# Kernel tuning notes

Measured on AMD Instinct MI355X. Metric: run time of the kernel, lower is better.

## Reference

```python
import jax, jax.numpy as jnp
from jax import lax
import numpy as np

EPS = 1e-5


def _fps(xyz, S):
    B, N, _ = xyz.shape

    def step(carry, _):
        dist, far = carry  # [B,N], [B]
        c = xyz[jnp.arange(B), far]               # [B,3]
        d = jnp.sum((xyz - c[:, None, :]) ** 2, -1)  # [B,N]
        dist = jnp.minimum(dist, d)
        nxt = jnp.argmax(dist, -1).astype(jnp.int32)
        return (dist, nxt), far

    init = (jnp.full((B, N), 1e10, xyz.dtype), jnp.zeros((B,), jnp.int32))
    _, idxs = lax.scan(step, init, None, length=S)
    return jnp.transpose(idxs)  # [B,S]


def _gather(pts, idx):
    # pts: [B,N,C], idx: [B,...] -> [B,...,C]
    return jax.vmap(lambda p, i: p[i])(pts, idx)


def _conv(x, W, b):
    # 1x1 Conv1d: x [M,Cin,L], W [Cout,Cin], b [Cout]
    return jnp.einsum('mcl,oc->mol', x, W) + b[None, :, None]


def _bn(x, g, b):
    # BatchNorm1d (training-mode batch stats, biased variance)
    mu = jnp.mean(x, (0, 2), keepdims=True)
    v = jnp.var(x, (0, 2), keepdims=True)
    return g[None, :, None] * (x - mu) / jnp.sqrt(v + EPS) + b[None, :, None]


def _forward(xyz, feature, affine_alpha, affine_beta, w_tr, b_tr, g_tr, be_tr,
             w1, b1, g1, be1, w2, b2, groups, k):
    xyz = jnp.transpose(xyz, (0, 2, 1))        # [B,N,3]
    feature = jnp.transpose(feature, (0, 2, 1))  # [B,N,D]
    B, N, _ = xyz.shape
    S = groups
    xyz_ng = lax.stop_gradient(xyz)  # cluster() runs under torch.no_grad
    fps_idx = _fps(xyz_ng, S)                        # [B,S]
    new_xyz = _gather(xyz_ng, fps_idx)               # [B,S,3] (detached)
    # squared-distance kNN: [B,S,N]
    sqr = (jnp.sum(new_xyz ** 2, -1)[:, :, None]
           + jnp.sum(xyz_ng ** 2, -1)[:, None, :]
           - 2.0 * jnp.einsum('bsc,bnc->bsn', new_xyz, xyz_ng))
    _, idx = lax.top_k(-sqr, k)                      # [B,S,k] smallest distances
    new_feature = _gather(feature, fps_idx)          # [B,S,D]
    grouped_xyz = _gather(xyz, idx)                  # [B,S,k,3]
    grouped_feature = _gather(feature, idx)          # [B,S,k,D]
    grouped_feature = jnp.concatenate([grouped_feature, grouped_xyz], -1)  # [B,S,k,D+3]
    # anchor normalization
    mean = jnp.concatenate([new_feature, new_xyz], -1)[:, :, None, :]  # [B,S,1,D+3]
    diff = grouped_feature - mean
    std = jnp.std(diff.reshape(B, -1), axis=-1, ddof=1)[:, None, None, None]
    gf = affine_alpha * (diff / (std + EPS)) + affine_beta
    # concat anchor feature -> [B,S,k,2D+3]
    D = new_feature.shape[-1]
    x = jnp.concatenate([gf, jnp.broadcast_to(new_feature[:, :, None, :], (B, S, k, D))], -1)
    d = x.shape[-1]
    # PreExtraction: [B,S,k,d] -> [B*S,d,k]
    x = jnp.transpose(x, (0, 1, 3, 2)).reshape(B * S, d, k)
    x = jax.nn.relu(_bn(_conv(x, w_tr, b_tr), g_tr, be_tr))
    y = jax.nn.relu(_bn(_conv(x, w1, b1), g1, be1))
    y = _conv(y, w2, b2)
    x = jax.nn.relu(y + x)
    x = jnp.max(x, -1).reshape(B, S, -1)             # adaptive_max_pool1d(1)
    return (jnp.transpose(new_xyz, (0, 2, 1)), jnp.transpose(x, (0, 2, 1)))


def setup_inputs() -> dict:
    key = jax.random.key(0)
    k0, k1, k2, k3, k4 = jax.random.split(key, 5)
    B, N, D = 8, 4096, 64
    return {
        'xyz': jax.random.normal(k0, (B, 3, N), jnp.float32),
        'feature': jax.random.normal(k1, (B, D, N), jnp.float32),
        'affine_alpha': jnp.ones((1, 1, 1, D + 3), jnp.float32),
        'affine_beta': jnp.zeros((1, 1, 1, D + 3), jnp.float32),
        'w_tr': 0.05 * jax.random.normal(k2, (D, 3 + 2 * D), jnp.float32),
        'b_tr': jnp.zeros((D,), jnp.float32),
        'g_tr': jnp.ones((D,), jnp.float32),
        'be_tr': jnp.zeros((D,), jnp.float32),
        'w1': 0.05 * jax.random.normal(k3, (D, D), jnp.float32),
        'b1': jnp.zeros((D,), jnp.float32),
        'g1': jnp.ones((D,), jnp.float32),
        'be1': jnp.zeros((D,), jnp.float32),
        'w2': 0.05 * jax.random.normal(k4, (D, D), jnp.float32),
        'b2': jnp.zeros((D,), jnp.float32),
        'groups': 1024,
        'k': 32,
    }


def reference(xyz, feature, affine_alpha, affine_beta, w_tr, b_tr, g_tr, be_tr,
              w1, b1, g1, be1, w2, b2, groups, k):
    return _forward(xyz, feature, affine_alpha, affine_beta, w_tr, b_tr, g_tr, be_tr,
                    w1, b1, g1, be1, w2, b2, groups, k)
```

## Files before the change

kernel.cpp:

```cpp
#include <hip/hip_runtime.h>
#include <cfloat>
#include <math.h>

#define B_ 8
#define N_ 4096
#define D_ 64
#define S_ 1024
#define K_ 32
#define CIN_ 131

template <int CTRL>
__device__ __forceinline__ unsigned long long dpp_u64(unsigned long long k) {
  int lo = (int)(unsigned int)k, hi = (int)(unsigned int)(k >> 32);
  lo = __builtin_amdgcn_update_dpp(lo, lo, CTRL, 0xf, 0xf, false);
  hi = __builtin_amdgcn_update_dpp(hi, hi, CTRL, 0xf, 0xf, false);
  return ((unsigned long long)(unsigned int)hi << 32) | (unsigned int)lo;
}

__device__ __forceinline__ float wave_max_f32_dpp(float v) {
  int x = __float_as_int(v);
#define STEP(ctrl)                                                        \
  {                                                                       \
    int t = __builtin_amdgcn_update_dpp(x, x, ctrl, 0xf, 0xf, false);     \
    v = fmaxf(v, __int_as_float(t));                                      \
    x = __float_as_int(v);                                                \
  }
  STEP(0x111)
  STEP(0x112)
  STEP(0x114)
  STEP(0x118)
  STEP(0x142)
  STEP(0x143)
#undef STEP
  return __int_as_float(__builtin_amdgcn_readlane(x, 63));
}

__global__ __launch_bounds__(512) void fps_kernel(const float* __restrict__ xyz,
                                                  int* __restrict__ fps_idx,
                                                  float* __restrict__ nxyz,
                                                  float* __restrict__ out0) {
  const int b = blockIdx.x, tid = threadIdx.x;
  __shared__ __align__(16) float4 sp[N_];
  __shared__ int si[S_];
  __shared__ unsigned long long keyp[2][8];
  const float* xb = xyz + (size_t)b * 3 * N_;
  const float4* xv = (const float4*)xb;
  float px[8], py[8], pz[8], dist[8];
  {
    float4 x0 = xv[2 * tid], x1 = xv[2 * tid + 1];
    float4 y0 = xv[1024 + 2 * tid], y1 = xv[1024 + 2 * tid + 1];
    float4 z0 = xv[2048 + 2 * tid], z1 = xv[2048 + 2 * tid + 1];
    px[0] = x0.x; px[1] = x0.y; px[2] = x0.z; px[3] = x0.w;
    px[4] = x1.x; px[5] = x1.y; px[6] = x1.z; px[7] = x1.w;
    py[0] = y0.x; py[1] = y0.y; py[2] = y0.z; py[3] = y0.w;
    py[4] = y1.x; py[5] = y1.y; py[6] = y1.z; py[7] = y1.w;
    pz[0] = z0.x; pz[1] = z0.y; pz[2] = z0.z; pz[3] = z0.w;
    pz[4] = z1.x; pz[5] = z1.y; pz[6] = z1.z; pz[7] = z1.w;
#pragma unroll
    for (int i = 0; i < 8; i++) {
      dist[i] = 1e10f;
      sp[8 * tid + i] = make_float4(px[i], py[i], pz[i], 0.f);
    }
  }
  if (tid == 0) si[0] = 0;
  __syncthreads();
  float cx = sp[0].x, cy = sp[0].y, cz = sp[0].z;
  const int wav = tid >> 6, lane = tid & 63;
  for (int s = 1; s < S_; s++) {
    float best = -1.0f;
    int bi = 8 * tid;
#pragma unroll
    for (int i = 0; i < 8; i++) {
      float dx = __fsub_rn(px[i], cx);
      float dy = __fsub_rn(py[i], cy);
      float dz = __fsub_rn(pz[i], cz);
      float d = __fadd_rn(__fadd_rn(__fmul_rn(dx, dx), __fmul_rn(dy, dy)), __fmul_rn(dz, dz));
      dist[i] = fminf(dist[i], d);
      if (dist[i] > best) { best = dist[i]; bi = 8 * tid + i; }
    }
    float wmax = wave_max_f32_dpp(best);
    unsigned long long m = __ballot(best == wmax);
    int l = __ffsll(m) - 1;
    int widx = __builtin_amdgcn_readlane(bi, l);
    if (lane == 0)
      keyp[s & 1][wav] =
          ((unsigned long long)(unsigned int)__float_as_int(wmax) << 32) |
          (unsigned int)(4095 - widx);
    __syncthreads();
    unsigned long long k = keyp[s & 1][lane & 7];
    unsigned long long t;
    t = dpp_u64<0xB1>(k);  if (t > k) k = t;
    t = dpp_u64<0x4E>(k);  if (t > k) k = t;
    t = dpp_u64<0x124>(k); if (t > k) k = t;
    int bix = 4095 - (int)(k & 0xfffull);
    if (tid == 0) si[s] = bix;
    float4 c = sp[bix];
    cx = c.x; cy = c.y; cz = c.z;
  }
  __syncthreads();
  for (int e = tid; e < S_; e += 512) {
    int n = si[e];
    fps_idx[b * S_ + e] = n;
    float4 c = sp[n];
    nxyz[(size_t)(b * S_ + e) * 3 + 0] = c.x;
    nxyz[(size_t)(b * S_ + e) * 3 + 1] = c.y;
    nxyz[(size_t)(b * S_ + e) * 3 + 2] = c.z;
    out0[(size_t)b * 3 * S_ + e] = c.x;
    out0[(size_t)b * 3 * S_ + S_ + e] = c.y;
    out0[(size_t)b * 3 * S_ + 2 * S_ + e] = c.z;
  }
}

__global__ __launch_bounds__(256) void knn_kernel(const float* __restrict__ xyz,
                                                  const float* __restrict__ nxyz,
                                                  int* __restrict__ knn) {
  const int bs = blockIdx.x, tid = threadIdx.x;
  const int b = bs >> 10;
  const float* xb = xyz + (size_t)b * 3 * N_;
  const float cx = nxyz[(size_t)bs * 3], cy = nxyz[(size_t)bs * 3 + 1], cz = nxyz[(size_t)bs * 3 + 2];
  const float cn = __fadd_rn(__fadd_rn(__fmul_rn(cx, cx), __fmul_rn(cy, cy)), __fmul_rn(cz, cz));
  float d[16];
#pragma unroll
  for (int i = 0; i < 16; i++) {
    int n = i * 256 + tid;
    float px = xb[n], py = xb[N_ + n], pz = xb[2 * N_ + n];
    float pn = __fadd_rn(__fadd_rn(__fmul_rn(px, px), __fmul_rn(py, py)), __fmul_rn(pz, pz));
    float dot = __fadd_rn(__fadd_rn(__fmul_rn(cx, px), __fmul_rn(cy, py)), __fmul_rn(cz, pz));
    d[i] = __fsub_rn(__fadd_rn(cn, pn), __fmul_rn(2.0f, dot));
  }
  float mv = FLT_MAX;
  int mi = tid;
#pragma unroll
  for (int i = 0; i < 16; i++)
    if (d[i] < mv) { mv = d[i]; mi = i * 256 + tid; }
  __shared__ unsigned long long keyp[2][4];
  __shared__ int skk[K_];
  const int wav = tid >> 6, lane = tid & 63;
  for (int j = 0; j < K_; j++) {
    unsigned int u = __float_as_uint(mv);
    u ^= ((unsigned int)((int)u >> 31) | 0x80000000u);
    unsigned long long key = ((unsigned long long)u << 32) | (unsigned int)mi;
#pragma unroll
    for (int off = 32; off >= 1; off >>= 1) {
      unsigned long long ok = __shfl_xor(key, off);
      if (ok < key) key = ok;
    }
    if (lane == 0) keyp[j & 1][wav] = key;
    __syncthreads();
    unsigned long long kmin = keyp[j & 1][0];
#pragma unroll
    for (int w = 1; w < 4; w++) {
      unsigned long long k2 = keyp[j & 1][w];
      if (k2 < kmin) kmin = k2;
    }
    int g = (int)(kmin & 0xffffffffull);
    if (tid == 0) skk[j] = g;
    if ((g & 255) == tid) {
      int sl = g >> 8;
#pragma unroll
      for (int i = 0; i < 16; i++)
        if (i == sl) d[i] = FLT_MAX;
      mv = FLT_MAX; mi = tid;
#pragma unroll
      for (int i = 0; i < 16; i++)
        if (d[i] < mv) { mv = d[i]; mi = i * 256 + tid; }
    }
  }
  __syncthreads();
  if (tid < K_) knn[(size_t)bs * K_ + tid] = skk[tid];
}

__global__ __launch_bounds__(256) void gather_nf(const float* __restrict__ feature,
                                                 const int* __restrict__ fps_i,
                                                 float* __restrict__ nfeat) {
  int e = blockIdx.x * 256 + threadIdx.x;
  int b = e >> 16, rem = e & 65535;
  int s = rem >> 6, c = rem & 63;
  int n = fps_i[b * S_ + s];
  nfeat[e] = feature[((size_t)b * 64 + c) * N_ + n];
}

__global__ __launch_bounds__(256) void std_partial(const float* __restrict__ feature,
                                                   const float* __restrict__ xyz,
                                                   const float* __restrict__ nxyz,
                                                   const float* __restrict__ nfeat,
                                                   const int* __restrict__ knn,
                                                   float* __restrict__ outp) {
  const int blk = blockIdx.x, tid = threadIdx.x;
  const int b = blk >> 6, chunk = blk & 63;
  float s = 0.f, q = 0.f;
  for (int e = tid; e < 16 * K_ * 67; e += 256) {
    int so = e / (K_ * 67);
    int rem = e - so * (K_ * 67);
    int kk = rem / 67;
    int c = rem - kk * 67;
    int bs = b * S_ + chunk * 16 + so;
    int n = knn[(size_t)bs * K_ + kk];
    float raw = (c < 64) ? feature[((size_t)b * 64 + c) * N_ + n]
                         : xyz[((size_t)b * 3 + (c - 64)) * N_ + n];
    float anc = (c < 64) ? nfeat[(size_t)bs * 64 + c]
                         : nxyz[(size_t)bs * 3 + (c - 64)];
    float dd = raw - anc;
    s += dd; q += dd * dd;
  }
#pragma unroll
  for (int off = 32; off >= 1; off >>= 1) { s += __shfl_xor(s, off); q += __shfl_xor(q, off); }
  __shared__ float rs[4], rq[4];
  if ((tid & 63) == 0) { rs[tid >> 6] = s; rq[tid >> 6] = q; }
  __syncthreads();
  if (tid == 0) {
    outp[blk * 2] = rs[0] + rs[1] + rs[2] + rs[3];
    outp[blk * 2 + 1] = rq[0] + rq[1] + rq[2] + rq[3];
  }
}

__global__ void std_final(const float* __restrict__ part, float* __restrict__ invstd) {
  int b = threadIdx.x;
  if (b < B_) {
    double s = 0.0, q = 0.0;
    for (int i = 0; i < 64; i++) {
      s += (double)part[(b * 64 + i) * 2];
      q += (double)part[(b * 64 + i) * 2 + 1];
    }
    const double n = (double)(S_ * K_ * 67);
    double var = (q - s * s / n) / (n - 1.0);
    invstd[b] = (float)(1.0 / (sqrt(var) + 1e-5));
  }
}

template <int MODE>
__global__ __launch_bounds__(256, 2) void mlp_kernel(
    const float* __restrict__ feature, const float* __restrict__ xyz,
    const float* __restrict__ nxyz, const float* __restrict__ nfeat,
    const int* __restrict__ knn, const float* __restrict__ invstd,
    const float* __restrict__ alpha, const float* __restrict__ beta,
    const float* __restrict__ w_tr, const float* __restrict__ b_tr,
    const float* __restrict__ w1, const float* __restrict__ b1,
    const float* __restrict__ w2, const float* __restrict__ b2,
    const float* __restrict__ bn_tr, const float* __restrict__ bn_1,
    float* __restrict__ bnpart, float* __restrict__ out1) {
  __shared__ __align__(16) float pool[15556];
  float* Wt = pool;
  float* xin = pool + 8516;
  float* ub = xin;
  float* tb = pool + 8516 + 4192;
  float* part = pool + 8516 + 4192 + 2304;
  int* sknn = (int*)(part + 512);
  const int bs = blockIdx.x, tid = threadIdx.x;
  const int b = bs >> 10, s = bs & 1023;
  if (tid < K_) sknn[tid] = knn[(size_t)bs * K_ + tid];
  for (int e = tid; e < 64 * 131; e += 256) {
    int o = e / 131, c = e - o * 131;
    Wt[c * 65 + o] = w_tr[e];
  }
  __syncthreads();
  const float inv = invstd[b];
  for (int e = tid; e < CIN_ * K_; e += 256) {
    int c = e >> 5, kk = e & 31;
    float v;
    if (c < 67) {
      int n = sknn[kk];
      float raw = (c < 64) ? feature[((size_t)b * 64 + c) * N_ + n]
                           : xyz[((size_t)b * 3 + (c - 64)) * N_ + n];
      float anc = (c < 64) ? nfeat[(size_t)bs * 64 + c]
                           : nxyz[(size_t)bs * 3 + (c - 64)];
      v = alpha[c] * ((raw - anc) * inv) + beta[c];
    } else {
      v = nfeat[(size_t)bs * 64 + (c - 67)];
    }
    xin[e] = v;
  }
  __syncthreads();
  const int o = tid & 63, kkb = (tid >> 6) * 8;
  float acc[8];
  {
    float bv = b_tr[o];
#pragma unroll
    for (int j = 0; j < 8; j++) acc[j] = bv;
  }
  for (int c = 0; c < CIN_; c++) {
    float w = Wt[c * 65 + o];
    const float4 xa = *(const float4*)(xin + c * 32 + kkb);
    const float4 xb4 = *(const float4*)(xin + c * 32 + kkb + 4);
    acc[0] += w * xa.x; acc[1] += w * xa.y; acc[2] += w * xa.z; acc[3] += w * xa.w;
    acc[4] += w * xb4.x; acc[5] += w * xb4.y; acc[6] += w * xb4.z; acc[7] += w * xb4.w;
  }
  if (MODE == 0) {
    float s8 = 0.f, q8 = 0.f;
#pragma unroll
    for (int j = 0; j < 8; j++) { s8 += acc[j]; q8 += acc[j] * acc[j]; }
    part[(tid >> 6) * 64 + o] = s8;
    part[256 + (tid >> 6) * 64 + o] = q8;
    __syncthreads();
    if (tid < 64) {
      float ss = 0.f, qq = 0.f;
      for (int g = 0; g < 4; g++) { ss += part[g * 64 + tid]; qq += part[256 + g * 64 + tid]; }
      bnpart[(size_t)bs * 128 + tid] = ss;
      bnpart[(size_t)bs * 128 + 64 + tid] = qq;
    }
    return;
  }
  float tv[8];
  {
    float sc = bn_tr[o], sh = bn_tr[64 + o];
#pragma unroll
    for (int j = 0; j < 8; j++) {
      tv[j] = fmaxf(fmaf(sc, acc[j], sh), 0.f);
      tb[o * 36 + kkb + j] = tv[j];
    }
  }
  __syncthreads();
  for (int e = tid; e < 64 * 64; e += 256) {
    int oo = e >> 6, c = e & 63;
    Wt[c * 65 + oo] = w1[e];
  }
  __syncthreads();
  float acc2[8];
  {
    float bv = b1[o];
#pragma unroll
    for (int j = 0; j < 8; j++) acc2[j] = bv;
  }
  for (int c = 0; c < 64; c++) {
    float w = Wt[c * 65 + o];
    const float4 ta = *(const float4*)(tb + c * 36 + kkb);
    const float4 ta2 = *(const float4*)(tb + c * 36 + kkb + 4);
    acc2[0] += w * ta.x; acc2[1] += w * ta.y; acc2[2] += w * ta.z; acc2[3] += w * ta.w;
    acc2[4] += w * ta2.x; acc2[5] += w * ta2.y; acc2[6] += w * ta2.z; acc2[7] += w * ta2.w;
  }
  if (MODE == 1) {
    float s8 = 0.f, q8 = 0.f;
#pragma unroll
    for (int j = 0; j < 8; j++) { s8 += acc2[j]; q8 += acc2[j] * acc2[j]; }
    part[(tid >> 6) * 64 + o] = s8;
    part[256 + (tid >> 6) * 64 + o] = q8;
    __syncthreads();
    if (tid < 64) {
      float ss = 0.f, qq = 0.f;
      for (int g = 0; g < 4; g++) { ss += part[g * 64 + tid]; qq += part[256 + g * 64 + tid]; }
      bnpart[(size_t)bs * 128 + tid] = ss;
      bnpart[(size_t)bs * 128 + 64 + tid] = qq;
    }
    return;
  }
  {
    float sc = bn_1[o], sh = bn_1[64 + o];
#pragma unroll
    for (int j = 0; j < 8; j++) ub[o * 36 + kkb + j] = fmaxf(fmaf(sc, acc2[j], sh), 0.f);
  }
  __syncthreads();
  for (int e = tid; e < 64 * 64; e += 256) {
    int oo = e >> 6, c = e & 63;
    Wt[c * 65 + oo] = w2[e];
  }
  __syncthreads();
  float acc3[8];
  {
    float bv = b2[o];
#pragma unroll
    for (int j = 0; j < 8; j++) acc3[j] = bv;
  }
  for (int c = 0; c < 64; c++) {
    float w = Wt[c * 65 + o];
    const float4 ua = *(const float4*)(ub + c * 36 + kkb);
    const float4 ua2 = *(const float4*)(ub + c * 36 + kkb + 4);
    acc3[0] += w * ua.x; acc3[1] += w * ua.y; acc3[2] += w * ua.z; acc3[3] += w * ua.w;
    acc3[4] += w * ua2.x; acc3[5] += w * ua2.y; acc3[6] += w * ua2.z; acc3[7] += w * ua2.w;
  }
  float m = 0.f;
#pragma unroll
  for (int j = 0; j < 8; j++) m = fmaxf(m, fmaxf(acc3[j] + tv[j], 0.f));
  part[(tid >> 6) * 64 + o] = m;
  __syncthreads();
  if (tid < 64) {
    float mm = part[tid];
    for (int g = 1; g < 4; g++) mm = fmaxf(mm, part[g * 64 + tid]);
    out1[((size_t)b * 64 + tid) * S_ + s] = mm;
  }
}

__global__ __launch_bounds__(256) void bn_finalize(const float* __restrict__ part,
                                                   const float* __restrict__ g,
                                                   const float* __restrict__ be,
                                                   float* __restrict__ bnout) {
  const int ch = blockIdx.x, tid = threadIdx.x;
  double s = 0.0, q = 0.0;
  for (int i = tid; i < B_ * S_; i += 256) {
    s += (double)part[(size_t)i * 128 + ch];
    q += (double)part[(size_t)i * 128 + 64 + ch];
  }
#pragma unroll
  for (int off = 32; off >= 1; off >>= 1) { s += __shfl_xor(s, off); q += __shfl_xor(q, off); }
  __shared__ double ls[4], lq[4];
  if ((tid & 63) == 0) { ls[tid >> 6] = s; lq[tid >> 6] = q; }
  __syncthreads();
  if (tid == 0) {
    double Ssum = ls[0] + ls[1] + ls[2] + ls[3];
    double Qsum = lq[0] + lq[1] + lq[2] + lq[3];
    const double n = (double)(B_ * S_ * K_);
    double mu = Ssum / n;
    double var = Qsum / n - mu * mu;
    double sc = (double)g[ch] / sqrt(var + 1e-5);
    bnout[ch] = (float)sc;
    bnout[64 + ch] = (float)((double)be[ch] - mu * sc);
  }
}


__global__ __launch_bounds__(256) void transpose_feat(const float* __restrict__ feature,
                                                      float* __restrict__ featT) {
  __shared__ float tile[64 * 65];
  const int blk = blockIdx.x, tid = threadIdx.x;
  const int b = blk >> 6, n0 = (blk & 63) * 64;
#pragma unroll
  for (int i = 0; i < 16; i++) {
    int c = i * 4 + (tid >> 6), nl = tid & 63;
    tile[c * 65 + nl] = feature[((size_t)b * 64 + c) * N_ + n0 + nl];
  }
  __syncthreads();
#pragma unroll
  for (int i = 0; i < 16; i++) {
    int nl = i * 4 + (tid >> 6), c = tid & 63;
    featT[((size_t)b * N_ + n0 + nl) * 64 + c] = tile[c * 65 + nl];
  }
}

__global__ __launch_bounds__(256) void gather_nf_c(const float* __restrict__ featT,
                                                   const int* __restrict__ fps_i,
                                                   float* __restrict__ nfeat) {
  int e = blockIdx.x * 256 + threadIdx.x;
  int bs = e >> 6, c = e & 63;
  int b = bs >> 10;
  int n = fps_i[bs];
  nfeat[e] = featT[((size_t)b * N_ + n) * 64 + c];
}

__global__ __launch_bounds__(256) void prep_kernel(const float* __restrict__ featT,
                                                   const float* __restrict__ xyz,
                                                   const float* __restrict__ nxyz,
                                                   const float* __restrict__ nfeat,
                                                   const int* __restrict__ knn,
                                                   float* __restrict__ dcache,
                                                   float* __restrict__ outp) {
  const int blk = blockIdx.x, tid = threadIdx.x;
  __shared__ int sk[32];
  float s = 0.f, q = 0.f;
  const int c = tid & 63, qd = tid >> 6;
  for (int g = 0; g < 8; g++) {
    const int bs = blk * 8 + g, b = bs >> 10;
    if (tid < 32) sk[tid] = knn[(size_t)bs * K_ + tid];
    __syncthreads();
    float anc = nfeat[(size_t)bs * 64 + c];
#pragma unroll
    for (int it = 0; it < 8; it++) {
      int kk = it * 4 + qd;
      int n = sk[kk];
      float dd = featT[((size_t)b * N_ + n) * 64 + c] - anc;
      s += dd; q += dd * dd;
      dcache[((size_t)bs * 32 + kk) * 68 + c] = dd;
    }
    if (tid < 96) {
      int c3 = tid >> 5, kk = tid & 31;
      int n = sk[kk];
      float dd = xyz[((size_t)b * 3 + c3) * N_ + n] - nxyz[(size_t)bs * 3 + c3];
      s += dd; q += dd * dd;
      dcache[((size_t)bs * 32 + kk) * 68 + 64 + c3] = dd;
    }
    __syncthreads();
  }
#pragma unroll
  for (int off = 32; off >= 1; off >>= 1) { s += __shfl_xor(s, off); q += __shfl_xor(q, off); }
  __shared__ float rs[4], rq[4];
  if ((tid & 63) == 0) { rs[tid >> 6] = s; rq[tid >> 6] = q; }
  __syncthreads();
  if (tid == 0) {
    outp[blk * 2] = rs[0] + rs[1] + rs[2] + rs[3];
    outp[blk * 2 + 1] = rq[0] + rq[1] + rq[2] + rq[3];
  }
}

__global__ void std_final_c(const float* __restrict__ part, float* __restrict__ invstd) {
  int b = threadIdx.x;
  if (b < B_) {
    double s = 0.0, q = 0.0;
    for (int i = 0; i < 128; i++) {
      s += (double)part[(b * 128 + i) * 2];
      q += (double)part[(b * 128 + i) * 2 + 1];
    }
    const double n = (double)(S_ * K_ * 67);
    double var = (q - s * s / n) / (n - 1.0);
    invstd[b] = (float)(1.0 / (sqrt(var) + 1e-5));
  }
}

__global__ __launch_bounds__(256, 2) void mlp0c(
    const float* __restrict__ dcache, const float* __restrict__ nfeat,
    const float* __restrict__ invstd,
    const float* __restrict__ alpha, const float* __restrict__ beta,
    const float* __restrict__ w_tr, const float* __restrict__ b_tr,
    float* __restrict__ bnpart, float* __restrict__ tcache) {
  __shared__ __align__(16) float pool[13220];
  float* Wt = pool;
  float* xin = pool + 8516;
  float* part = pool + 8516 + 4192;
  const int bs = blockIdx.x, tid = threadIdx.x;
  const int b = bs >> 10;
  for (int e = tid; e < 64 * 131; e += 256) {
    int o = e / 131, c = e - o * 131;
    Wt[c * 65 + o] = w_tr[e];
  }
  const float inv = invstd[b];
  {
    const int c = tid & 63, qd = tid >> 6;
    float al = alpha[c], bev = beta[c];
#pragma unroll
    for (int it = 0; it < 8; it++) {
      int kk = it * 4 + qd;
      xin[c * 32 + kk] = al * (dcache[((size_t)bs * 32 + kk) * 68 + c] * inv) + bev;
    }
    if (tid < 96) {
      int c3 = 64 + (tid >> 5), kk = tid & 31;
      xin[c3 * 32 + kk] =
          alpha[c3] * (dcache[((size_t)bs * 32 + kk) * 68 + c3] * inv) + beta[c3];
    }
    for (int e = tid; e < 2048; e += 256) {
      int cc = 67 + (e >> 5), kk = e & 31;
      xin[cc * 32 + kk] = nfeat[(size_t)bs * 64 + (e >> 5)];
    }
  }
  __syncthreads();
  const int o = tid & 63, kkb = (tid >> 6) * 8;
  float acc[8];
  {
    float bv = b_tr[o];
#pragma unroll
    for (int j = 0; j < 8; j++) acc[j] = bv;
  }
  for (int c = 0; c < CIN_; c++) {
    float w = Wt[c * 65 + o];
    const float4 xa = *(const float4*)(xin + c * 32 + kkb);
    const float4 xb4 = *(const float4*)(xin + c * 32 + kkb + 4);
    acc[0] += w * xa.x; acc[1] += w * xa.y; acc[2] += w * xa.z; acc[3] += w * xa.w;
    acc[4] += w * xb4.x; acc[5] += w * xb4.y; acc[6] += w * xb4.z; acc[7] += w * xb4.w;
  }
  {
    float4* tp = (float4*)(tcache + ((size_t)bs * 64 + o) * 32 + kkb);
    tp[0] = make_float4(acc[0], acc[1], acc[2], acc[3]);
    tp[1] = make_float4(acc[4], acc[5], acc[6], acc[7]);
  }
  float s8 = 0.f, q8 = 0.f;
#pragma unroll
  for (int j = 0; j < 8; j++) { s8 += acc[j]; q8 += acc[j] * acc[j]; }
  part[(tid >> 6) * 64 + o] = s8;
  part[256 + (tid >> 6) * 64 + o] = q8;
  __syncthreads();
  if (tid < 64) {
    float ss = 0.f, qq = 0.f;
    for (int g = 0; g < 4; g++) { ss += part[g * 64 + tid]; qq += part[256 + g * 64 + tid]; }
    bnpart[(size_t)bs * 128 + tid] = ss;
    bnpart[(size_t)bs * 128 + 64 + tid] = qq;
  }
}

__global__ __launch_bounds__(256, 3) void mlp1c(
    const float* __restrict__ tcache, const float* __restrict__ bn_tr,
    const float* __restrict__ w1, const float* __restrict__ b1,
    float* __restrict__ bnpart, float* __restrict__ ucache) {
  __shared__ __align__(16) float pool[6976];
  float* Wt = pool;
  float* tb = pool + 4160;
  float* part = pool + 4160 + 2304;
  const int bs = blockIdx.x, tid = threadIdx.x;
  const int o = tid & 63, kkb = (tid >> 6) * 8;
  for (int e = tid; e < 64 * 64; e += 256) {
    int oo = e >> 6, c = e & 63;
    Wt[c * 65 + oo] = w1[e];
  }
  float t[8];
  {
    const float4* tp = (const float4*)(tcache + ((size_t)bs * 64 + o) * 32 + kkb);
    float4 a = tp[0], b4 = tp[1];
    t[0] = a.x; t[1] = a.y; t[2] = a.z; t[3] = a.w;
    t[4] = b4.x; t[5] = b4.y; t[6] = b4.z; t[7] = b4.w;
  }
  {
    float sc = bn_tr[o], sh = bn_tr[64 + o];
#pragma unroll
    for (int j = 0; j < 8; j++) tb[o * 36 + kkb + j] = fmaxf(fmaf(sc, t[j], sh), 0.f);
  }
  __syncthreads();
  float acc2[8];
  {
    float bv = b1[o];
#pragma unroll
    for (int j = 0; j < 8; j++) acc2[j] = bv;
  }
  for (int c = 0; c < 64; c++) {
    float w = Wt[c * 65 + o];
    const float4 ta = *(const float4*)(tb + c * 36 + kkb);
    const float4 ta2 = *(const float4*)(tb + c * 36 + kkb + 4);
    acc2[0] += w * ta.x; acc2[1] += w * ta.y; acc2[2] += w * ta.z; acc2[3] += w * ta.w;
    acc2[4] += w * ta2.x; acc2[5] += w * ta2.y; acc2[6] += w * ta2.z; acc2[7] += w * ta2.w;
  }
  {
    float4* up = (float4*)(ucache + ((size_t)bs * 64 + o) * 32 + kkb);
    up[0] = make_float4(acc2[0], acc2[1], acc2[2], acc2[3]);
    up[1] = make_float4(acc2[4], acc2[5], acc2[6], acc2[7]);
  }
  float s8 = 0.f, q8 = 0.f;
#pragma unroll
  for (int j = 0; j < 8; j++) { s8 += acc2[j]; q8 += acc2[j] * acc2[j]; }
  part[(tid >> 6) * 64 + o] = s8;
  part[256 + (tid >> 6) * 64 + o] = q8;
  __syncthreads();
  if (tid < 64) {
    float ss = 0.f, qq = 0.f;
    for (int g = 0; g < 4; g++) { ss += part[g * 64 + tid]; qq += part[256 + g * 64 + tid]; }
    bnpart[(size_t)bs * 128 + tid] = ss;
    bnpart[(size_t)bs * 128 + 64 + tid] = qq;
  }
}

__global__ __launch_bounds__(256, 3) void mlp2c(
    const float* __restrict__ tcache, const float* __restrict__ ucache,
    const float* __restrict__ bn_tr, const float* __restrict__ bn_1,
    const float* __restrict__ w2, const float* __restrict__ b2,
    float* __restrict__ out1) {
  __shared__ __align__(16) float pool[6976];
  float* Wt = pool;
  float* ub = pool + 4160;
  float* part = pool + 4160 + 2304;
  const int bs = blockIdx.x, tid = threadIdx.x;
  const int b = bs >> 10, s = bs & 1023;
  const int o = tid & 63, kkb = (tid >> 6) * 8;
  for (int e = tid; e < 64 * 64; e += 256) {
    int oo = e >> 6, c = e & 63;
    Wt[c * 65 + oo] = w2[e];
  }
  {
    const float4* up = (const float4*)(ucache + ((size_t)bs * 64 + o) * 32 + kkb);
    float4 a = up[0], b4 = up[1];
    float u[8] = {a.x, a.y, a.z, a.w, b4.x, b4.y, b4.z, b4.w};
    float sc = bn_1[o], sh = bn_1[64 + o];
#pragma unroll
    for (int j = 0; j < 8; j++) ub[o * 36 + kkb + j] = fmaxf(fmaf(sc, u[j], sh), 0.f);
  }
  __syncthreads();
  float acc3[8];
  {
    float bv = b2[o];
#pragma unroll
    for (int j = 0; j < 8; j++) acc3[j] = bv;
  }
  for (int c = 0; c < 64; c++) {
    float w = Wt[c * 65 + o];
    const float4 ua = *(const float4*)(ub + c * 36 + kkb);
    const float4 ua2 = *(const float4*)(ub + c * 36 + kkb + 4);
    acc3[0] += w * ua.x; acc3[1] += w * ua.y; acc3[2] += w * ua.z; acc3[3] += w * ua.w;
    acc3[4] += w * ua2.x; acc3[5] += w * ua2.y; acc3[6] += w * ua2.z; acc3[7] += w * ua2.w;
  }
  float tv[8];
  {
    const float4* tp = (const float4*)(tcache + ((size_t)bs * 64 + o) * 32 + kkb);
    float4 a = tp[0], b4 = tp[1];
    float t[8] = {a.x, a.y, a.z, a.w, b4.x, b4.y, b4.z, b4.w};
    float sc = bn_tr[o], sh = bn_tr[64 + o];
#pragma unroll
    for (int j = 0; j < 8; j++) tv[j] = fmaxf(fmaf(sc, t[j], sh), 0.f);
  }
  float m = 0.f;
#pragma unroll
  for (int j = 0; j < 8; j++) m = fmaxf(m, fmaxf(acc3[j] + tv[j], 0.f));
  part[(tid >> 6) * 64 + o] = m;
  __syncthreads();
  if (tid < 64) {
    float mm = part[tid];
    for (int g = 1; g < 4; g++) mm = fmaxf(mm, part[g * 64 + tid]);
    out1[((size_t)b * 64 + tid) * S_ + s] = mm;
  }
}

extern "C" void kernel_launch(void* const* d_in, const int* in_sizes, int n_in,
                              void* d_out, int out_size, void* d_ws, size_t ws_size,
                              hipStream_t stream) {
  const float* xyz = (const float*)d_in[0];
  const float* feature = (const float*)d_in[1];
  const float* alpha = (const float*)d_in[2];
  const float* beta = (const float*)d_in[3];
  const float* w_tr = (const float*)d_in[4];
  const float* b_tr = (const float*)d_in[5];
  const float* g_tr = (const float*)d_in[6];
  const float* be_tr = (const float*)d_in[7];
  const float* w1 = (const float*)d_in[8];
  const float* b1 = (const float*)d_in[9];
  const float* g1 = (const float*)d_in[10];
  const float* be1 = (const float*)d_in[11];
  const float* w2 = (const float*)d_in[12];
  const float* b2 = (const float*)d_in[13];

  char* ws = (char*)d_ws;
  int* fps_i = (int*)(ws);
  float* nxyz = (float*)(ws + 32768);
  float* nfeat = (float*)(ws + 131072);
  int* knn = (int*)(ws + 2228224);
  float* stdpart = (float*)(ws + 3276800);
  float* invstd = (float*)(ws + 3280896);
  float* bn_tr = (float*)(ws + 3280960);
  float* bn_1 = (float*)(ws + 3281472);
  float* bnpart = (float*)(ws + 3281984);
  float* featT = (float*)(ws + 7476288);
  float* dcache = (float*)(ws + 15864896);
  float* tcache = (float*)(ws + 87168064);
  float* ucache = (float*)(ws + 154276928);
  float* stdpart_c = (float*)(ws + 221385792);

  float* out0 = (float*)d_out;
  float* out1 = out0 + B_ * 3 * S_;

  const bool big = (ws_size >= 221393984ull);

  fps_kernel<<<B_, 512, 0, stream>>>(xyz, fps_i, nxyz, out0);

  if (big) {
    transpose_feat<<<8 * 64, 256, 0, stream>>>(feature, featT);
    knn_kernel<<<B_ * S_, 256, 0, stream>>>(xyz, nxyz, knn);
    gather_nf_c<<<(B_ * S_ * D_) / 256, 256, 0, stream>>>(featT, fps_i, nfeat);
    prep_kernel<<<1024, 256, 0, stream>>>(featT, xyz, nxyz, nfeat, knn, dcache, stdpart_c);
    std_final_c<<<1, 64, 0, stream>>>(stdpart_c, invstd);
    mlp0c<<<B_ * S_, 256, 0, stream>>>(dcache, nfeat, invstd, alpha, beta, w_tr, b_tr,
                                       bnpart, tcache);
    bn_finalize<<<64, 256, 0, stream>>>(bnpart, g_tr, be_tr, bn_tr);
    mlp1c<<<B_ * S_, 256, 0, stream>>>(tcache, bn_tr, w1, b1, bnpart, ucache);
    bn_finalize<<<64, 256, 0, stream>>>(bnpart, g1, be1, bn_1);
    mlp2c<<<B_ * S_, 256, 0, stream>>>(tcache, ucache, bn_tr, bn_1, w2, b2, out1);
  } else {
    gather_nf<<<(B_ * S_ * D_) / 256, 256, 0, stream>>>(feature, fps_i, nfeat);
    knn_kernel<<<B_ * S_, 256, 0, stream>>>(xyz, nxyz, knn);
    std_partial<<<B_ * 64, 256, 0, stream>>>(feature, xyz, nxyz, nfeat, knn, stdpart);
    std_final<<<1, 64, 0, stream>>>(stdpart, invstd);
    mlp_kernel<0><<<B_ * S_, 256, 0, stream>>>(feature, xyz, nxyz, nfeat, knn, invstd,
                                               alpha, beta, w_tr, b_tr, w1, b1, w2, b2,
                                               bn_tr, bn_1, bnpart, out1);
    bn_finalize<<<64, 256, 0, stream>>>(bnpart, g_tr, be_tr, bn_tr);
    mlp_kernel<1><<<B_ * S_, 256, 0, stream>>>(feature, xyz, nxyz, nfeat, knn, invstd,
                                               alpha, beta, w_tr, b_tr, w1, b1, w2, b2,
                                               bn_tr, bn_1, bnpart, out1);
    bn_finalize<<<64, 256, 0, stream>>>(bnpart, g1, be1, bn_1);
    mlp_kernel<2><<<B_ * S_, 256, 0, stream>>>(feature, xyz, nxyz, nfeat, knn, invstd,
                                               alpha, beta, w_tr, b_tr, w1, b1, w2, b2,
                                               bn_tr, bn_1, bnpart, out1);
  }
}
```

Baseline: 1.196 ms.

## Fuse feature transpose into FPS launch and gather into kNN launch, shrink FPS block

```diff
diff --git a/kernel.cpp b/kernel.cpp
--- a/kernel.cpp
+++ b/kernel.cpp
@@ -35,32 +35,50 @@
   return __int_as_float(__builtin_amdgcn_readlane(x, 63));
 }
 
-__global__ __launch_bounds__(512) void fps_kernel(const float* __restrict__ xyz,
+__global__ __launch_bounds__(256) void fps_kernel(const float* __restrict__ xyz,
                                                   int* __restrict__ fps_idx,
                                                   float* __restrict__ nxyz,
-                                                  float* __restrict__ out0) {
-  const int b = blockIdx.x, tid = threadIdx.x;
+                                                  float* __restrict__ out0,
+                                                  const float* __restrict__ feature,
+                                                  float* __restrict__ featT) {
+  const int tid = threadIdx.x;
   __shared__ __align__(16) float4 sp[N_];
   __shared__ int si[S_];
-  __shared__ unsigned long long keyp[2][8];
+  __shared__ unsigned long long keyp[2][4];
+  if (blockIdx.x >= 8) {
+    const int blk = blockIdx.x - 8;
+    const int b = blk >> 6, n0 = (blk & 63) * 64;
+    float* tile = (float*)sp;
+#pragma unroll
+    for (int i = 0; i < 16; i++) {
+      int c = i * 4 + (tid >> 6), nl = tid & 63;
+      tile[c * 65 + nl] = feature[((size_t)b * 64 + c) * N_ + n0 + nl];
+    }
+    __syncthreads();
+#pragma unroll
+    for (int i = 0; i < 16; i++) {
+      int nl = i * 4 + (tid >> 6), c = tid & 63;
+      featT[((size_t)b * N_ + n0 + nl) * 64 + c] = tile[c * 65 + nl];
+    }
+    return;
+  }
+  const int b = blockIdx.x;
   const float* xb = xyz + (size_t)b * 3 * N_;
   const float4* xv = (const float4*)xb;
-  float px[8], py[8], pz[8], dist[8];
-  {
-    float4 x0 = xv[2 * tid], x1 = xv[2 * tid + 1];
-    float4 y0 = xv[1024 + 2 * tid], y1 = xv[1024 + 2 * tid + 1];
-    float4 z0 = xv[2048 + 2 * tid], z1 = xv[2048 + 2 * tid + 1];
-    px[0] = x0.x; px[1] = x0.y; px[2] = x0.z; px[3] = x0.w;
-    px[4] = x1.x; px[5] = x1.y; px[6] = x1.z; px[7] = x1.w;
-    py[0] = y0.x; py[1] = y0.y; py[2] = y0.z; py[3] = y0.w;
-    py[4] = y1.x; py[5] = y1.y; py[6] = y1.z; py[7] = y1.w;
-    pz[0] = z0.x; pz[1] = z0.y; pz[2] = z0.z; pz[3] = z0.w;
-    pz[4] = z1.x; pz[5] = z1.y; pz[6] = z1.z; pz[7] = z1.w;
-#pragma unroll
-    for (int i = 0; i < 8; i++) {
-      dist[i] = 1e10f;
-      sp[8 * tid + i] = make_float4(px[i], py[i], pz[i], 0.f);
-    }
+  float px[16], py[16], pz[16], dist[16];
+#pragma unroll
+  for (int q = 0; q < 4; q++) {
+    float4 X = xv[4 * tid + q];
+    float4 Y = xv[1024 + 4 * tid + q];
+    float4 Z = xv[2048 + 4 * tid + q];
+    px[4 * q + 0] = X.x; px[4 * q + 1] = X.y; px[4 * q + 2] = X.z; px[4 * q + 3] = X.w;
+    py[4 * q + 0] = Y.x; py[4 * q + 1] = Y.y; py[4 * q + 2] = Y.z; py[4 * q + 3] = Y.w;
+    pz[4 * q + 0] = Z.x; pz[4 * q + 1] = Z.y; pz[4 * q + 2] = Z.z; pz[4 * q + 3] = Z.w;
+  }
+#pragma unroll
+  for (int i = 0; i < 16; i++) {
+    dist[i] = 1e10f;
+    sp[16 * tid + i] = make_float4(px[i], py[i], pz[i], 0.f);
   }
   if (tid == 0) si[0] = 0;
   __syncthreads();
@@ -68,15 +86,15 @@
   const int wav = tid >> 6, lane = tid & 63;
   for (int s = 1; s < S_; s++) {
     float best = -1.0f;
-    int bi = 8 * tid;
-#pragma unroll
-    for (int i = 0; i < 8; i++) {
+    int bi = 16 * tid;
+#pragma unroll
+    for (int i = 0; i < 16; i++) {
       float dx = __fsub_rn(px[i], cx);
       float dy = __fsub_rn(py[i], cy);
       float dz = __fsub_rn(pz[i], cz);
       float d = __fadd_rn(__fadd_rn(__fmul_rn(dx, dx), __fmul_rn(dy, dy)), __fmul_rn(dz, dz));
       dist[i] = fminf(dist[i], d);
-      if (dist[i] > best) { best = dist[i]; bi = 8 * tid + i; }
+      if (dist[i] > best) { best = dist[i]; bi = 16 * tid + i; }
     }
     float wmax = wave_max_f32_dpp(best);
     unsigned long long m = __ballot(best == wmax);
@@ -87,18 +105,17 @@
           ((unsigned long long)(unsigned int)__float_as_int(wmax) << 32) |
           (unsigned int)(4095 - widx);
     __syncthreads();
-    unsigned long long k = keyp[s & 1][lane & 7];
+    unsigned long long k = keyp[s & 1][lane & 3];
     unsigned long long t;
-    t = dpp_u64<0xB1>(k);  if (t > k) k = t;
-    t = dpp_u64<0x4E>(k);  if (t > k) k = t;
-    t = dpp_u64<0x124>(k); if (t > k) k = t;
+    t = dpp_u64<0xB1>(k); if (t > k) k = t;
+    t = dpp_u64<0x4E>(k); if (t > k) k = t;
     int bix = 4095 - (int)(k & 0xfffull);
     if (tid == 0) si[s] = bix;
     float4 c = sp[bix];
     cx = c.x; cy = c.y; cz = c.z;
   }
   __syncthreads();
-  for (int e = tid; e < S_; e += 512) {
+  for (int e = tid; e < S_; e += 256) {
     int n = si[e];
     fps_idx[b * S_ + e] = n;
     float4 c = sp[n];
@@ -113,8 +130,19 @@
 
 __global__ __launch_bounds__(256) void knn_kernel(const float* __restrict__ xyz,
                                                   const float* __restrict__ nxyz,
-                                                  int* __restrict__ knn) {
+                                                  int* __restrict__ knn,
+                                                  const float* __restrict__ featT,
+                                                  const int* __restrict__ fps_i,
+                                                  float* __restrict__ nfeat) {
   const int bs = blockIdx.x, tid = threadIdx.x;
+  if (bs >= 8192) {
+    int e = (bs - 8192) * 256 + tid;
+    int bsx = e >> 6, c = e & 63;
+    int bq = bsx >> 10;
+    int n = fps_i[bsx];
+    nfeat[e] = featT[((size_t)bq * N_ + n) * 64 + c];
+    return;
+  }
   const int b = bs >> 10;
   const float* xb = xyz + (size_t)b * 3 * N_;
   const float cx = nxyz[(size_t)bs * 3], cy = nxyz[(size_t)bs * 3 + 1], cz = nxyz[(size_t)bs * 3 + 2];
@@ -407,34 +435,6 @@
 }
 
 
-__global__ __launch_bounds__(256) void transpose_feat(const float* __restrict__ feature,
-                                                      float* __restrict__ featT) {
-  __shared__ float tile[64 * 65];
-  const int blk = blockIdx.x, tid = threadIdx.x;
-  const int b = blk >> 6, n0 = (blk & 63) * 64;
-#pragma unroll
-  for (int i = 0; i < 16; i++) {
-    int c = i * 4 + (tid >> 6), nl = tid & 63;
-    tile[c * 65 + nl] = feature[((size_t)b * 64 + c) * N_ + n0 + nl];
-  }
-  __syncthreads();
-#pragma unroll
-  for (int i = 0; i < 16; i++) {
-    int nl = i * 4 + (tid >> 6), c = tid & 63;
-    featT[((size_t)b * N_ + n0 + nl) * 64 + c] = tile[c * 65 + nl];
-  }
-}
-
-__global__ __launch_bounds__(256) void gather_nf_c(const float* __restrict__ featT,
-                                                   const int* __restrict__ fps_i,
-                                                   float* __restrict__ nfeat) {
-  int e = blockIdx.x * 256 + threadIdx.x;
-  int bs = e >> 6, c = e & 63;
-  int b = bs >> 10;
-  int n = fps_i[bs];
-  nfeat[e] = featT[((size_t)b * N_ + n) * 64 + c];
-}
-
 __global__ __launch_bounds__(256) void prep_kernel(const float* __restrict__ featT,
                                                    const float* __restrict__ xyz,
                                                    const float* __restrict__ nxyz,
@@ -719,12 +719,9 @@
 
   const bool big = (ws_size >= 221393984ull);
 
-  fps_kernel<<<B_, 512, 0, stream>>>(xyz, fps_i, nxyz, out0);
-
   if (big) {
-    transpose_feat<<<8 * 64, 256, 0, stream>>>(feature, featT);
-    knn_kernel<<<B_ * S_, 256, 0, stream>>>(xyz, nxyz, knn);
-    gather_nf_c<<<(B_ * S_ * D_) / 256, 256, 0, stream>>>(featT, fps_i, nfeat);
+    fps_kernel<<<8 + 512, 256, 0, stream>>>(xyz, fps_i, nxyz, out0, feature, featT);
+    knn_kernel<<<8192 + 2048, 256, 0, stream>>>(xyz, nxyz, knn, featT, fps_i, nfeat);
     prep_kernel<<<1024, 256, 0, stream>>>(featT, xyz, nxyz, nfeat, knn, dcache, stdpart_c);
     std_final_c<<<1, 64, 0, stream>>>(stdpart_c, invstd);
     mlp0c<<<B_ * S_, 256, 0, stream>>>(dcache, nfeat, invstd, alpha, beta, w_tr, b_tr,
@@ -734,8 +731,9 @@
     bn_finalize<<<64, 256, 0, stream>>>(bnpart, g1, be1, bn_1);
     mlp2c<<<B_ * S_, 256, 0, stream>>>(tcache, ucache, bn_tr, bn_1, w2, b2, out1);
   } else {
+    fps_kernel<<<8, 256, 0, stream>>>(xyz, fps_i, nxyz, out0, feature, featT);
     gather_nf<<<(B_ * S_ * D_) / 256, 256, 0, stream>>>(feature, fps_i, nfeat);
-    knn_kernel<<<B_ * S_, 256, 0, stream>>>(xyz, nxyz, knn);
+    knn_kernel<<<8192, 256, 0, stream>>>(xyz, nxyz, knn, nullptr, nullptr, nullptr);
     std_partial<<<B_ * 64, 256, 0, stream>>>(feature, xyz, nxyz, nfeat, knn, stdpart);
     std_final<<<1, 64, 0, stream>>>(stdpart, invstd);
     mlp_kernel<0><<<B_ * S_, 256, 0, stream>>>(feature, xyz, nxyz, nfeat, knn, invstd,
```

After: 1.167 ms (median of 2 runs). 1.03x faster.
